# Kernel tuning notes

Hardware: AMD Instinct MI355X
Metric: run time of the kernel (lower is better)

The kernel has to match this reference:

```python
import jax, jax.numpy as jnp
import numpy as np

B, H, E = 32, 128, 64           # batch, hidden_size, embedding_size
D, N, P = 32, 512, 8            # max_depth, nodes per depth, max parents
TOTAL = 2 + D * N               # padding slot + root slot + all DAG nodes


def setup_inputs() -> dict:
    key = jax.random.key(0)
    ks = jax.random.split(key, 6)
    embedding = jax.random.normal(ks[0], (B, H), dtype=jnp.float32)
    emb_table = jax.random.normal(ks[1], (TOTAL, E), dtype=jnp.float32) * 0.1
    emb_table = emb_table.at[0].set(0.0)  # padding_idx=0
    W1 = jax.random.normal(ks[2], (H, H + E), dtype=jnp.float32) * (1.0 / np.sqrt(H + E))
    b1 = jax.random.normal(ks[3], (H,), dtype=jnp.float32) * 0.01
    W2 = jax.random.normal(ks[4], (H, H), dtype=jnp.float32) * (1.0 / np.sqrt(H))
    b2 = jax.random.normal(ks[5], (H,), dtype=jnp.float32) * 0.01
    # Synthetic rooted DAG: depth-d nodes' parents are any earlier slot in [1, 1+d*N].
    rng = np.random.default_rng(0)
    pidx = np.zeros((D, N, P), dtype=np.int32)
    for d in range(D):
        hi = 2 + d * N  # exclusive upper bound of valid parent slots
        pidx[d] = rng.integers(1, hi, size=(N, P))
        mask = rng.random((N, P)) < 0.3
        mask[:, 0] = False  # every node keeps at least one parent
        pidx[d][mask] = 0
    parent_idx = jnp.asarray(pidx)
    return {"embedding": embedding, "emb_table": emb_table, "W1": W1, "b1": b1,
            "W2": W2, "b2": b2, "parent_idx": parent_idx}


def reference(embedding, emb_table, W1, b1, W2, b2, parent_idx):
    dt = embedding.dtype
    # node_vecs buffer: slot 0 = padding(zeros), slot 1 = root embedding
    buf = jnp.zeros((B, TOTAL, H), dtype=dt).at[:, 1, :].set(embedding)
    # embedding-table indices of depth-d nodes: 2 + d*N + arange(N)
    node_idx = 2 + jnp.arange(D, dtype=jnp.int32)[:, None] * N \
                 + jnp.arange(N, dtype=jnp.int32)[None, :]          # [D, N]

    def step(buf, xs):
        pidx, nidx, d = xs                                          # [N,P], [N], scalar
        # gather parent vectors and sum over the parent axis
        pv = buf[:, pidx.reshape(-1), :].reshape(B, N, P, H).sum(axis=2)  # [B,N,H]
        ne = jnp.broadcast_to(emb_table[nidx], (B, N, E))           # [B,N,E]
        x = jnp.concatenate([pv, ne], axis=-1)                      # [B,N,H+E]
        h = jax.nn.relu(jnp.einsum('bnf,hf->bnh', x, W1) + b1)
        h = jnp.einsum('bnf,hf->bnh', h, W2) + b2
        v = pv + h                                                  # residual
        buf = jax.lax.dynamic_update_slice(buf, v.astype(dt), (0, 2 + d * N, 0))
        return buf, None

    buf, _ = jax.lax.scan(step, buf, (parent_idx, node_idx,
                                      jnp.arange(D, dtype=jnp.int32)))
    return buf[:, 1:, :]                                            # [B, 1+D*N, H]
```

## Files before the change

### kernel.cpp

```cpp
#include <hip/hip_runtime.h>
#include <hip/hip_cooperative_groups.h>

namespace cg = cooperative_groups;

#define BATCH 32
#define HID   128
#define EMB   64
#define DEPTHS 32
#define NODES 512
#define PAR   8
#define OUTROWS 16385
#define ROWSTRIDE ((size_t)OUTROWS * HID)

typedef short bf16x8 __attribute__((ext_vector_type(8)));
typedef float f32x4  __attribute__((ext_vector_type(4)));

#define WS_W1L 24576
#define WS_W2H 49152
#define WS_W2L 65536
#define WS_BYTES 163840

__device__ __forceinline__ void split1(float x, unsigned short& h, unsigned short& l) {
    unsigned u  = __float_as_uint(x);
    unsigned hu = u & 0xFFFF0000u;
    h = (unsigned short)(hu >> 16);
    float r = x - __uint_as_float(hu);
    l = (unsigned short)(__float_as_uint(r) >> 16);
}

__global__ void __launch_bounds__(256) init_kernel(const float* __restrict__ emb,
                                                   float* __restrict__ out) {
    int i = blockIdx.x * 256 + threadIdx.x;
    int b = i >> 7, h = i & 127;
    out[(size_t)b * ROWSTRIDE + h] = emb[i];
}

__global__ void __launch_bounds__(256) prep_kernel(const float* __restrict__ W1f,
                                                   const float* __restrict__ W2f,
                                                   unsigned short* __restrict__ wsw) {
    int i = blockIdx.x * 256 + threadIdx.x;
    unsigned short h, l;
    if (i < 24576) {
        split1(W1f[i], h, l);
        wsw[i] = h; wsw[WS_W1L + i] = l;
    } else {
        int j = i - 24576;
        split1(W2f[j], h, l);
        wsw[WS_W2H + j] = h; wsw[WS_W2L + j] = l;
    }
}

__device__ __forceinline__ void depth_body(
    char* smem,
    float* __restrict__ bbase,
    const float* __restrict__ emb_table,
    const float* __restrict__ W1f,
    const float* __restrict__ b1,
    const float* __restrict__ W2f,
    const float* __restrict__ b2,
    const int*   __restrict__ parent_idx,
    const unsigned short* __restrict__ wsw,
    int d, int n0, int use_ws, int t)
{
    float* xs = (float*)smem;

    {
        const int lane = t & 31, rsub = t >> 5;
        for (int rr = rsub; rr < 16; rr += 8) {
            const int* pp = parent_idx + ((d << 9) + n0 + rr) * PAR;
            float4 a = make_float4(0.f, 0.f, 0.f, 0.f);
            #pragma unroll
            for (int p = 0; p < PAR; ++p) {
                const int s = pp[p];
                if (s > 0) {
                    const float4 v = *(const float4*)(bbase + (size_t)(s - 1) * HID + lane * 4);
                    a.x += v.x; a.y += v.y; a.z += v.z; a.w += v.w;
                }
            }
            *(float4*)&xs[rr * 204 + lane * 4] = a;
        }
        const int base_row = 2 + (d << 9) + n0;
        const int r = t >> 4, e4 = t & 15;
        *(float4*)&xs[r * 204 + 128 + e4 * 4] =
            *(const float4*)(emb_table + (size_t)(base_row + r) * EMB + e4 * 4);
    }
    __syncthreads();

    unsigned short* xh = (unsigned short*)(smem + 13056);
    unsigned short* xl = xh + 16 * 216;
    {
        const int r = t >> 4, cs = (t & 15) * 12;
        #pragma unroll
        for (int j = 0; j < 12; ++j) {
            unsigned short h, l;
            split1(xs[r * 204 + cs + j], h, l);
            xh[r * 216 + cs + j] = h;
            xl[r * 216 + cs + j] = l;
        }
    }
    __syncthreads();

    const int lane = t & 63, w = t >> 6;
    const int quad = lane >> 4, nib = lane & 15;

    f32x4 acc1[2] = {{0.f,0.f,0.f,0.f},{0.f,0.f,0.f,0.f}};
    for (int k0 = 0; k0 < 192; k0 += 32) {
        const int ko = k0 + quad * 8;
        const bf16x8 ah = *(const bf16x8*)(xh + nib * 216 + ko);
        const bf16x8 al = *(const bf16x8*)(xl + nib * 216 + ko);
        #pragma unroll
        for (int nt = 0; nt < 2; ++nt) {
            const int n = ((w << 1) + nt) * 16 + nib;
            bf16x8 bh, bl;
            if (use_ws) {
                bh = *(const bf16x8*)(wsw + n * 192 + ko);
                bl = *(const bf16x8*)(wsw + WS_W1L + n * 192 + ko);
            } else {
                const float4 f0 = *(const float4*)(W1f + n * 192 + ko);
                const float4 f1 = *(const float4*)(W1f + n * 192 + ko + 4);
                const float ff[8] = {f0.x,f0.y,f0.z,f0.w,f1.x,f1.y,f1.z,f1.w};
                #pragma unroll
                for (int j = 0; j < 8; ++j) {
                    unsigned short hq, lq; split1(ff[j], hq, lq);
                    bh[j] = (short)hq; bl[j] = (short)lq;
                }
            }
            acc1[nt] = __builtin_amdgcn_mfma_f32_16x16x32_bf16(ah, bh, acc1[nt], 0, 0, 0);
            acc1[nt] = __builtin_amdgcn_mfma_f32_16x16x32_bf16(ah, bl, acc1[nt], 0, 0, 0);
            acc1[nt] = __builtin_amdgcn_mfma_f32_16x16x32_bf16(al, bh, acc1[nt], 0, 0, 0);
        }
    }
    __syncthreads();

    unsigned short* hh = (unsigned short*)(smem + 13056);
    unsigned short* hl = hh + 16 * 136;
    #pragma unroll
    for (int nt = 0; nt < 2; ++nt) {
        const int c = ((w << 1) + nt) * 16 + nib;
        const float bb = b1[c];
        #pragma unroll
        for (int reg = 0; reg < 4; ++reg) {
            const int r = quad * 4 + reg;
            float h = fmaxf(acc1[nt][reg] + bb, 0.f);
            unsigned short hq, lq; split1(h, hq, lq);
            hh[r * 136 + c] = hq;
            hl[r * 136 + c] = lq;
        }
    }
    __syncthreads();

    f32x4 acc2[2] = {{0.f,0.f,0.f,0.f},{0.f,0.f,0.f,0.f}};
    for (int k0 = 0; k0 < 128; k0 += 32) {
        const int ko = k0 + quad * 8;
        const bf16x8 ah = *(const bf16x8*)(hh + nib * 136 + ko);
        const bf16x8 al = *(const bf16x8*)(hl + nib * 136 + ko);
        #pragma unroll
        for (int nt = 0; nt < 2; ++nt) {
            const int n = ((w << 1) + nt) * 16 + nib;
            bf16x8 bh, bl;
            if (use_ws) {
                bh = *(const bf16x8*)(wsw + WS_W2H + n * 128 + ko);
                bl = *(const bf16x8*)(wsw + WS_W2L + n * 128 + ko);
            } else {
                const float4 f0 = *(const float4*)(W2f + n * 128 + ko);
                const float4 f1 = *(const float4*)(W2f + n * 128 + ko + 4);
                const float ff[8] = {f0.x,f0.y,f0.z,f0.w,f1.x,f1.y,f1.z,f1.w};
                #pragma unroll
                for (int j = 0; j < 8; ++j) {
                    unsigned short hq, lq; split1(ff[j], hq, lq);
                    bh[j] = (short)hq; bl[j] = (short)lq;
                }
            }
            acc2[nt] = __builtin_amdgcn_mfma_f32_16x16x32_bf16(ah, bh, acc2[nt], 0, 0, 0);
            acc2[nt] = __builtin_amdgcn_mfma_f32_16x16x32_bf16(ah, bl, acc2[nt], 0, 0, 0);
            acc2[nt] = __builtin_amdgcn_mfma_f32_16x16x32_bf16(al, bh, acc2[nt], 0, 0, 0);
        }
    }
    __syncthreads();

    float* os = (float*)(smem + 13056);
    #pragma unroll
    for (int nt = 0; nt < 2; ++nt) {
        const int c = ((w << 1) + nt) * 16 + nib;
        const float bb = b2[c];
        #pragma unroll
        for (int reg = 0; reg < 4; ++reg) {
            const int r = quad * 4 + reg;
            os[r * 132 + c] = acc2[nt][reg] + bb;
        }
    }
    __syncthreads();

    {
        const int r = t >> 4, c = (t & 15) * 8;
        float4 o0 = *(float4*)&os[r * 132 + c];
        float4 o1 = *(float4*)&os[r * 132 + c + 4];
        const float4 p0 = *(const float4*)&xs[r * 204 + c];
        const float4 p1 = *(const float4*)&xs[r * 204 + c + 4];
        o0.x += p0.x; o0.y += p0.y; o0.z += p0.z; o0.w += p0.w;
        o1.x += p1.x; o1.y += p1.y; o1.z += p1.z; o1.w += p1.w;
        float* dst = bbase + (size_t)(1 + (d << 9) + n0 + r) * HID + c;
        *(float4*)dst = o0;
        *(float4*)(dst + 4) = o1;
    }
}

__device__ __forceinline__ int swizzle_wg(int bid) {
    return ((bid & 7) << 7) + (bid >> 3);
}

__global__ void __launch_bounds__(256) depth_kernel(
    float* __restrict__ buf, const float* __restrict__ emb_table,
    const float* __restrict__ W1f, const float* __restrict__ b1,
    const float* __restrict__ W2f, const float* __restrict__ b2,
    const int* __restrict__ parent_idx, const unsigned short* __restrict__ wsw,
    int d, int use_ws)
{
    __shared__ __align__(16) char smem[13056 + 13824];
    const int swz = swizzle_wg(blockIdx.x);
    const int b   = swz >> 5;
    const int n0  = (swz & 31) << 4;
    float* __restrict__ bbase = buf + (size_t)b * ROWSTRIDE;
    depth_body(smem, bbase, emb_table, W1f, b1, W2f, b2, parent_idx, wsw,
               d, n0, use_ws, threadIdx.x);
}

__global__ void __launch_bounds__(256, 4) depth_all_kernel(
    float* __restrict__ buf, const float* __restrict__ emb_table,
    const float* __restrict__ W1f, const float* __restrict__ b1,
    const float* __restrict__ W2f, const float* __restrict__ b2,
    const int* __restrict__ parent_idx, const unsigned short* __restrict__ wsw,
    int use_ws)
{
    cg::grid_group grid = cg::this_grid();
    __shared__ __align__(16) char smem[13056 + 13824];
    const int t   = threadIdx.x;
    const int swz = swizzle_wg(blockIdx.x);
    const int b   = swz >> 5;
    const int n0  = (swz & 31) << 4;
    float* __restrict__ bbase = buf + (size_t)b * ROWSTRIDE;

    for (int d = 0; d < DEPTHS; ++d) {
        if (d) grid.sync();
        depth_body(smem, bbase, emb_table, W1f, b1, W2f, b2, parent_idx, wsw,
                   d, n0, use_ws, t);
    }
}

extern "C" void kernel_launch(void* const* d_in, const int* in_sizes, int n_in,
                              void* d_out, int out_size, void* d_ws, size_t ws_size,
                              hipStream_t stream) {
    const float* embedding  = (const float*)d_in[0];
    const float* emb_table  = (const float*)d_in[1];
    const float* W1         = (const float*)d_in[2];
    const float* b1         = (const float*)d_in[3];
    const float* W2         = (const float*)d_in[4];
    const float* b2         = (const float*)d_in[5];
    const int*   parent_idx = (const int*)d_in[6];
    float* out = (float*)d_out;
    unsigned short* wsw = (unsigned short*)d_ws;
    int use_ws = (ws_size >= (size_t)WS_BYTES) ? 1 : 0;

    init_kernel<<<16, 256, 0, stream>>>(embedding, out);
    if (use_ws) prep_kernel<<<160, 256, 0, stream>>>(W1, W2, wsw);

    static int coop_ok = -1;
    if (coop_ok < 0) {
        int nb = 0;
        hipError_t e = hipOccupancyMaxActiveBlocksPerMultiprocessor(
            &nb, depth_all_kernel, 256, 0);
        coop_ok = (e == hipSuccess && nb >= 4) ? 1 : 0;
    }

    bool launched = false;
    if (coop_ok) {
        void* args[] = {(void*)&out, (void*)&emb_table, (void*)&W1, (void*)&b1,
                        (void*)&W2, (void*)&b2, (void*)&parent_idx, (void*)&wsw,
                        (void*)&use_ws};
        hipError_t e = hipLaunchCooperativeKernel(
            (const void*)depth_all_kernel, dim3(1024), dim3(256), args, 0, stream);
        launched = (e == hipSuccess);
        if (!launched) coop_ok = 0;
    }
    if (!launched) {
        for (int d = 0; d < DEPTHS; ++d) {
            depth_kernel<<<1024, 256, 0, stream>>>(out, emb_table, W1, b1, W2, b2,
                                                   parent_idx, wsw, d, use_ws);
        }
    }
}
```

Baseline: 1.181 ms.

## Add slot-major workspace path with precomputed embedding projection and per-node blocks

Adds a fast path that keeps a slot-major copy of node vectors in the workspace so the 32 batch rows of a parent slot sit next to each other. Each block handles one node and 16 batch rows, and the embedding half of the first layer (emb_table·W1b + b1) is precomputed once for all nodes, so the per-depth GEMM only covers K=128. The cooperative single-kernel grid-sync path is dropped for 32 separate launches. The fast path needs about 270 MB of workspace, writes every result twice (workspace and output), and pays launch overhead per depth.

```diff
diff --git a/kernel.cpp b/kernel.cpp
--- a/kernel.cpp
+++ b/kernel.cpp
@@ -1,7 +1,4 @@
 #include <hip/hip_runtime.h>
-#include <hip/hip_cooperative_groups.h>
-
-namespace cg = cooperative_groups;
 
 #define BATCH 32
 #define HID   128
@@ -11,6 +8,7 @@
 #define PAR   8
 #define OUTROWS 16385
 #define ROWSTRIDE ((size_t)OUTROWS * HID)
+#define TOTALSLOTS 16386
 
 typedef short bf16x8 __attribute__((ext_vector_type(8)));
 typedef float f32x4  __attribute__((ext_vector_type(4)));
@@ -19,6 +17,14 @@
 #define WS_W2H 49152
 #define WS_W2L 65536
 #define WS_BYTES 163840
+
+#define FW_W1AH 0u
+#define FW_W1AL 32768u
+#define FW_W2H  65536u
+#define FW_W2L  98304u
+#define FW_EP   131072u
+#define FW_WB   (131072u + 8388608u)
+#define FW_BYTES ((size_t)FW_WB + (size_t)TOTALSLOTS * BATCH * HID * 4)
 
 __device__ __forceinline__ void split1(float x, unsigned short& h, unsigned short& l) {
     unsigned u  = __float_as_uint(x);
@@ -27,6 +33,198 @@
     float r = x - __uint_as_float(hu);
     l = (unsigned short)(__float_as_uint(r) >> 16);
 }
+
+
+__global__ void __launch_bounds__(256) init_fast_kernel(const float* __restrict__ emb,
+                                                        float* __restrict__ out,
+                                                        float* __restrict__ wb) {
+    int i = blockIdx.x * 256 + threadIdx.x;
+    int b = i >> 7, h = i & 127;
+    float v = emb[i];
+    out[(size_t)b * ROWSTRIDE + h] = v;
+    wb[(size_t)(BATCH + b) * HID + h] = v;
+}
+
+__global__ void __launch_bounds__(256) prep_w_fast(const float* __restrict__ W1f,
+                                                   const float* __restrict__ W2f,
+                                                   char* __restrict__ ws) {
+    int i = blockIdx.x * 256 + threadIdx.x;
+    unsigned short h, l;
+    split1(W1f[(i >> 7) * 192 + (i & 127)], h, l);
+    ((unsigned short*)(ws + FW_W1AH))[i] = h;
+    ((unsigned short*)(ws + FW_W1AL))[i] = l;
+    split1(W2f[i], h, l);
+    ((unsigned short*)(ws + FW_W2H))[i] = h;
+    ((unsigned short*)(ws + FW_W2L))[i] = l;
+}
+
+__global__ void __launch_bounds__(256) prep_e_fast(const float* __restrict__ emb_table,
+                                                   const float* __restrict__ W1f,
+                                                   const float* __restrict__ b1,
+                                                   float* __restrict__ ep) {
+    __shared__ float semb[16 * 64];
+    __shared__ float swT[64 * 129];
+    const int t  = threadIdx.x;
+    const int nb = blockIdx.x * 16;
+    ((float4*)semb)[t] = ((const float4*)(emb_table + (size_t)(2 + nb) * EMB))[t];
+    for (int q = t; q < 8192; q += 256) {
+        const int c = q >> 6, e = q & 63;
+        swT[e * 129 + c] = W1f[c * 192 + 128 + e];
+    }
+    __syncthreads();
+    #pragma unroll
+    for (int u = 0; u < 8; ++u) {
+        const int q = t + 256 * u;
+        const int r = q >> 7, c = q & 127;
+        float acc = b1[c];
+        #pragma unroll 4
+        for (int e = 0; e < 64; ++e)
+            acc += semb[r * 64 + e] * swT[e * 129 + c];
+        ep[(size_t)(nb + r) * HID + c] = acc;
+    }
+}
+
+__global__ void __launch_bounds__(256, 4) depth_fast_kernel(
+    float* __restrict__ out,
+    const int* __restrict__ parent_idx,
+    const float* __restrict__ b2,
+    char* __restrict__ ws, int d)
+{
+    __shared__ __align__(16) char smem[8448 + 8704];
+    float* xs = (float*)smem;
+
+    const int t   = threadIdx.x;
+    const int bid = blockIdx.x;
+    const int swz = ((bid & 7) << 7) + (bid >> 3);
+    const int n   = swz >> 1;
+    const int bo  = (swz & 1) << 4;
+    float* __restrict__ wb = (float*)(ws + FW_WB);
+
+    {
+        const int q = (((d << 9) + n) << 3);
+        const int4 pa = *(const int4*)(parent_idx + q);
+        const int4 pb = *(const int4*)(parent_idx + q + 4);
+        const int sarr[8] = {pa.x, pa.y, pa.z, pa.w, pb.x, pb.y, pb.z, pb.w};
+        f32x4 a0 = {0.f,0.f,0.f,0.f}, a1 = {0.f,0.f,0.f,0.f};
+        #pragma unroll
+        for (int p = 0; p < PAR; ++p) {
+            const int s = sarr[p];
+            if (s > 0) {
+                const float* base = wb + ((size_t)s * BATCH + bo) * HID;
+                const f32x4 v0 = *(const f32x4*)(base + (t << 2));
+                const f32x4 v1 = *(const f32x4*)(base + 1024 + (t << 2));
+                a0 += v0; a1 += v1;
+            }
+        }
+        const int r0 = t >> 5, c0 = (t & 31) << 2;
+        *(f32x4*)&xs[r0 * 132 + c0]       = a0;
+        *(f32x4*)&xs[(r0 + 8) * 132 + c0] = a1;
+    }
+    __syncthreads();
+
+    unsigned short* xh = (unsigned short*)(smem + 8448);
+    unsigned short* xl = xh + 16 * 136;
+    {
+        const int r = t >> 4, cs = (t & 15) << 3;
+        #pragma unroll
+        for (int j = 0; j < 8; ++j) {
+            unsigned short h, l;
+            split1(xs[r * 132 + cs + j], h, l);
+            xh[r * 136 + cs + j] = h;
+            xl[r * 136 + cs + j] = l;
+        }
+    }
+    __syncthreads();
+
+    const int lane = t & 63, w = t >> 6;
+    const int quad = lane >> 4, nib = lane & 15;
+
+    const unsigned short* w1h = (const unsigned short*)(ws + FW_W1AH);
+    const unsigned short* w1l = (const unsigned short*)(ws + FW_W1AL);
+    f32x4 acc1[2] = {{0.f,0.f,0.f,0.f},{0.f,0.f,0.f,0.f}};
+    for (int k0 = 0; k0 < 128; k0 += 32) {
+        const int ko = k0 + quad * 8;
+        const bf16x8 ah = *(const bf16x8*)(xh + nib * 136 + ko);
+        const bf16x8 al = *(const bf16x8*)(xl + nib * 136 + ko);
+        #pragma unroll
+        for (int nt = 0; nt < 2; ++nt) {
+            const int c = ((w << 1) + nt) * 16 + nib;
+            const bf16x8 bh = *(const bf16x8*)(w1h + c * 128 + ko);
+            const bf16x8 bl = *(const bf16x8*)(w1l + c * 128 + ko);
+            acc1[nt] = __builtin_amdgcn_mfma_f32_16x16x32_bf16(ah, bh, acc1[nt], 0, 0, 0);
+            acc1[nt] = __builtin_amdgcn_mfma_f32_16x16x32_bf16(ah, bl, acc1[nt], 0, 0, 0);
+            acc1[nt] = __builtin_amdgcn_mfma_f32_16x16x32_bf16(al, bh, acc1[nt], 0, 0, 0);
+        }
+    }
+    __syncthreads();
+
+    unsigned short* hh = xh;
+    unsigned short* hl = xl;
+    const float* __restrict__ epn = (const float*)(ws + FW_EP) + (size_t)((d << 9) + n) * HID;
+    #pragma unroll
+    for (int nt = 0; nt < 2; ++nt) {
+        const int c = ((w << 1) + nt) * 16 + nib;
+        const float bb = epn[c];
+        #pragma unroll
+        for (int reg = 0; reg < 4; ++reg) {
+            const int r = quad * 4 + reg;
+            float h = fmaxf(acc1[nt][reg] + bb, 0.f);
+            unsigned short hq, lq; split1(h, hq, lq);
+            hh[r * 136 + c] = hq;
+            hl[r * 136 + c] = lq;
+        }
+    }
+    __syncthreads();
+
+    const unsigned short* w2h = (const unsigned short*)(ws + FW_W2H);
+    const unsigned short* w2l = (const unsigned short*)(ws + FW_W2L);
+    f32x4 acc2[2] = {{0.f,0.f,0.f,0.f},{0.f,0.f,0.f,0.f}};
+    for (int k0 = 0; k0 < 128; k0 += 32) {
+        const int ko = k0 + quad * 8;
+        const bf16x8 ah = *(const bf16x8*)(hh + nib * 136 + ko);
+        const bf16x8 al = *(const bf16x8*)(hl + nib * 136 + ko);
+        #pragma unroll
+        for (int nt = 0; nt < 2; ++nt) {
+            const int c = ((w << 1) + nt) * 16 + nib;
+            const bf16x8 bh = *(const bf16x8*)(w2h + c * 128 + ko);
+            const bf16x8 bl = *(const bf16x8*)(w2l + c * 128 + ko);
+            acc2[nt] = __builtin_amdgcn_mfma_f32_16x16x32_bf16(ah, bh, acc2[nt], 0, 0, 0);
+            acc2[nt] = __builtin_amdgcn_mfma_f32_16x16x32_bf16(ah, bl, acc2[nt], 0, 0, 0);
+            acc2[nt] = __builtin_amdgcn_mfma_f32_16x16x32_bf16(al, bh, acc2[nt], 0, 0, 0);
+        }
+    }
+    __syncthreads();
+
+    float* os = (float*)(smem + 8448);
+    #pragma unroll
+    for (int nt = 0; nt < 2; ++nt) {
+        const int c = ((w << 1) + nt) * 16 + nib;
+        const float bb = b2[c];
+        #pragma unroll
+        for (int reg = 0; reg < 4; ++reg) {
+            const int r = quad * 4 + reg;
+            os[r * 132 + c] = acc2[nt][reg] + bb;
+        }
+    }
+    __syncthreads();
+
+    {
+        const int r = t >> 4, c = (t & 15) << 3;
+        f32x4 o0 = *(f32x4*)&os[r * 132 + c];
+        f32x4 o1 = *(f32x4*)&os[r * 132 + c + 4];
+        o0 += *(const f32x4*)&xs[r * 132 + c];
+        o1 += *(const f32x4*)&xs[r * 132 + c + 4];
+        const size_t slot = (size_t)2 + (d << 9) + n;
+        float* dwb = wb + (slot * BATCH + bo + r) * HID + c;
+        *(f32x4*)dwb = o0;
+        *(f32x4*)(dwb + 4) = o1;
+        float* dou = out + (size_t)(bo + r) * ROWSTRIDE
+                         + ((size_t)1 + (d << 9) + n) * HID + c;
+        *(f32x4*)dou = o0;
+        *(f32x4*)(dou + 4) = o1;
+    }
+}
+
 
 __global__ void __launch_bounds__(256) init_kernel(const float* __restrict__ emb,
                                                    float* __restrict__ out) {
@@ -50,19 +248,20 @@
     }
 }
 
-__device__ __forceinline__ void depth_body(
-    char* smem,
-    float* __restrict__ bbase,
-    const float* __restrict__ emb_table,
-    const float* __restrict__ W1f,
-    const float* __restrict__ b1,
-    const float* __restrict__ W2f,
-    const float* __restrict__ b2,
-    const int*   __restrict__ parent_idx,
-    const unsigned short* __restrict__ wsw,
-    int d, int n0, int use_ws, int t)
+__global__ void __launch_bounds__(256) depth_kernel(
+    float* __restrict__ buf, const float* __restrict__ emb_table,
+    const float* __restrict__ W1f, const float* __restrict__ b1,
+    const float* __restrict__ W2f, const float* __restrict__ b2,
+    const int* __restrict__ parent_idx, const unsigned short* __restrict__ wsw,
+    int d, int use_ws)
 {
+    __shared__ __align__(16) char smem[13056 + 13824];
     float* xs = (float*)smem;
+    const int t   = threadIdx.x;
+    const int swz = ((blockIdx.x & 7) << 7) + (blockIdx.x >> 3);
+    const int b   = swz >> 5;
+    const int n0  = (swz & 31) << 4;
+    float* __restrict__ bbase = buf + (size_t)b * ROWSTRIDE;
 
     {
         const int lane = t & 31, rsub = t >> 5;
@@ -205,47 +404,6 @@
     }
 }
 
-__device__ __forceinline__ int swizzle_wg(int bid) {
-    return ((bid & 7) << 7) + (bid >> 3);
-}
-
-__global__ void __launch_bounds__(256) depth_kernel(
-    float* __restrict__ buf, const float* __restrict__ emb_table,
-    const float* __restrict__ W1f, const float* __restrict__ b1,
-    const float* __restrict__ W2f, const float* __restrict__ b2,
-    const int* __restrict__ parent_idx, const unsigned short* __restrict__ wsw,
-    int d, int use_ws)
-{
-    __shared__ __align__(16) char smem[13056 + 13824];
-    const int swz = swizzle_wg(blockIdx.x);
-    const int b   = swz >> 5;
-    const int n0  = (swz & 31) << 4;
-    float* __restrict__ bbase = buf + (size_t)b * ROWSTRIDE;
-    depth_body(smem, bbase, emb_table, W1f, b1, W2f, b2, parent_idx, wsw,
-               d, n0, use_ws, threadIdx.x);
-}
-
-__global__ void __launch_bounds__(256, 4) depth_all_kernel(
-    float* __restrict__ buf, const float* __restrict__ emb_table,
-    const float* __restrict__ W1f, const float* __restrict__ b1,
-    const float* __restrict__ W2f, const float* __restrict__ b2,
-    const int* __restrict__ parent_idx, const unsigned short* __restrict__ wsw,
-    int use_ws)
-{
-    cg::grid_group grid = cg::this_grid();
-    __shared__ __align__(16) char smem[13056 + 13824];
-    const int t   = threadIdx.x;
-    const int swz = swizzle_wg(blockIdx.x);
-    const int b   = swz >> 5;
-    const int n0  = (swz & 31) << 4;
-    float* __restrict__ bbase = buf + (size_t)b * ROWSTRIDE;
-
-    for (int d = 0; d < DEPTHS; ++d) {
-        if (d) grid.sync();
-        depth_body(smem, bbase, emb_table, W1f, b1, W2f, b2, parent_idx, wsw,
-                   d, n0, use_ws, t);
-    }
-}
 
 extern "C" void kernel_launch(void* const* d_in, const int* in_sizes, int n_in,
                               void* d_out, int out_size, void* d_ws, size_t ws_size,
@@ -258,31 +416,20 @@
     const float* b2         = (const float*)d_in[5];
     const int*   parent_idx = (const int*)d_in[6];
     float* out = (float*)d_out;
-    unsigned short* wsw = (unsigned short*)d_ws;
-    int use_ws = (ws_size >= (size_t)WS_BYTES) ? 1 : 0;
-
-    init_kernel<<<16, 256, 0, stream>>>(embedding, out);
-    if (use_ws) prep_kernel<<<160, 256, 0, stream>>>(W1, W2, wsw);
-
-    static int coop_ok = -1;
-    if (coop_ok < 0) {
-        int nb = 0;
-        hipError_t e = hipOccupancyMaxActiveBlocksPerMultiprocessor(
-            &nb, depth_all_kernel, 256, 0);
-        coop_ok = (e == hipSuccess && nb >= 4) ? 1 : 0;
-    }
-
-    bool launched = false;
-    if (coop_ok) {
-        void* args[] = {(void*)&out, (void*)&emb_table, (void*)&W1, (void*)&b1,
-                        (void*)&W2, (void*)&b2, (void*)&parent_idx, (void*)&wsw,
-                        (void*)&use_ws};
-        hipError_t e = hipLaunchCooperativeKernel(
-            (const void*)depth_all_kernel, dim3(1024), dim3(256), args, 0, stream);
-        launched = (e == hipSuccess);
-        if (!launched) coop_ok = 0;
-    }
-    if (!launched) {
+
+    if (ws_size >= FW_BYTES) {
+        char* ws = (char*)d_ws;
+        init_fast_kernel<<<16, 256, 0, stream>>>(embedding, out, (float*)(ws + FW_WB));
+        prep_w_fast<<<64, 256, 0, stream>>>(W1, W2, ws);
+        prep_e_fast<<<1024, 256, 0, stream>>>(emb_table, W1, b1, (float*)(ws + FW_EP));
+        for (int d = 0; d < DEPTHS; ++d) {
+            depth_fast_kernel<<<1024, 256, 0, stream>>>(out, parent_idx, b2, ws, d);
+        }
+    } else {
+        unsigned short* wsw = (unsigned short*)d_ws;
+        const int use_ws = (ws_size >= (size_t)WS_BYTES) ? 1 : 0;
+        init_kernel<<<16, 256, 0, stream>>>(embedding, out);
+        if (use_ws) prep_kernel<<<160, 256, 0, stream>>>(W1, W2, wsw);
         for (int d = 0; d < DEPTHS; ++d) {
             depth_kernel<<<1024, 256, 0, stream>>>(out, emb_table, W1, b1, W2, b2,
                                                    parent_idx, wsw, d, use_ws);
```

Measured after the change: 1.074 ms. 9.1% less time.
